# Kernel tuning notes

Hardware: AMD Instinct MI355X
Metric: run time of the kernel (lower is better)

The kernel has to match this reference:

```python
import jax, jax.numpy as jnp
import numpy as np

B, IN, H, M = 16384, 512, 512, 4096


def setup_inputs() -> dict:
    key = jax.random.key(0)
    ks = jax.random.split(key, 8)
    s_in = 1.0 / np.sqrt(IN + H)
    return {
        "input_tensor": jax.random.normal(ks[0], (B, IN), jnp.float32),
        "hidden": jax.random.normal(ks[1], (B, H), jnp.float32),
        "cell": jax.random.normal(ks[2], (B, H), jnp.float32),
        # fused gate weights: columns = [input, forget, cell, output] gates
        "W_gates": jax.random.normal(ks[3], (IN + H, 4 * H), jnp.float32) * s_in,
        "b_gates": jnp.zeros((4 * H,), jnp.float32),
        "W_attn": jax.random.normal(ks[4], (H, M), jnp.float32) / np.sqrt(H),
        "b_attn": jnp.zeros((M,), jnp.float32),
        "memory_matrix": jax.random.normal(ks[5], (M, H), jnp.float32) * np.sqrt(2.0 / (M + H)),
    }


def reference(input_tensor, hidden, cell, W_gates, b_gates, W_attn, b_attn, memory_matrix):
    combined = jnp.concatenate([input_tensor, hidden], axis=1)        # (B, IN+H)
    gates = combined @ W_gates + b_gates                              # (B, 4H)
    i_g, f_g, c_g, o_g = jnp.split(gates, 4, axis=1)
    i_g = jax.nn.sigmoid(i_g)
    f_g = jax.nn.sigmoid(f_g)
    c_g = jnp.tanh(c_g)
    o_g = jax.nn.sigmoid(o_g)
    attn = jax.nn.softmax(hidden @ W_attn + b_attn, axis=1)           # (B, M)
    memory_read = attn @ memory_matrix                                # (B, H)
    new_cell = f_g * cell + i_g * c_g + 0.1 * memory_read
    new_hidden = o_g * jnp.tanh(new_cell)
    return (new_hidden, new_cell, attn)
```

## Files before the change

kernel.cpp:

```cpp
#include <hip/hip_runtime.h>
#include <hip/hip_bf16.h>
#include <math.h>

typedef __bf16 bf16_t;
typedef bf16_t bf16x8 __attribute__((ext_vector_type(8)));
typedef float  f32x4  __attribute__((ext_vector_type(4)));

static constexpr int Bn = 16384;
static constexpr int Hn = 512;

__device__ __forceinline__ float sigm(float x) { return 1.0f / (1.0f + __expf(-x)); }

typedef __attribute__((address_space(3))) void lds_void;
typedef const __attribute__((address_space(1))) void gl_void;

__device__ __forceinline__ void glds16(const void* g, void* l) {
    __builtin_amdgcn_global_load_lds((gl_void*)g, (lds_void*)l, 16, 0, 0);
}

__global__ void convert_comb(const float* __restrict__ inp, const float* __restrict__ hid,
                             bf16_t* __restrict__ comb)
{
    size_t t = (size_t)blockIdx.x * blockDim.x + threadIdx.x;
    size_t r = t >> 7;
    int c8 = (int)(t & 127);
    const float* src = (c8 < 64) ? (inp + r * 512 + c8 * 8) : (hid + r * 512 + (c8 - 64) * 8);
    float4 a = ((const float4*)src)[0];
    float4 b = ((const float4*)src)[1];
    bf16x8 o;
    o[0] = (bf16_t)a.x; o[1] = (bf16_t)a.y; o[2] = (bf16_t)a.z; o[3] = (bf16_t)a.w;
    o[4] = (bf16_t)b.x; o[5] = (bf16_t)b.y; o[6] = (bf16_t)b.z; o[7] = (bf16_t)b.w;
    *(bf16x8*)(comb + t * 8) = o;
}

__global__ void transpose_all(const float* __restrict__ Wg, bf16_t* __restrict__ WgT,
                              const float* __restrict__ Wa, bf16_t* __restrict__ WaT,
                              const float* __restrict__ Mem, bf16_t* __restrict__ MemT)
{
    __shared__ float tile[32][33];
    int b = blockIdx.x;
    const float* src; bf16_t* dst; int R, C, gx;
    if (b < 2048)      { src = Wg;  dst = WgT;  R = 1024; C = 2048; gx = 64; }
    else if (b < 4096) { b -= 2048; src = Wa;  dst = WaT;  R = 512;  C = 4096; gx = 128; }
    else               { b -= 4096; src = Mem; dst = MemT; R = 4096; C = 512;  gx = 16; }
    const int x0 = (b % gx) * 32, y0 = (b / gx) * 32;
    const int tx = threadIdx.x & 31, ty = threadIdx.x >> 5;
#pragma unroll
    for (int i = 0; i < 32; i += 8)
        tile[ty + i][tx] = src[(size_t)(y0 + ty + i) * C + x0 + tx];
    __syncthreads();
#pragma unroll
    for (int i = 0; i < 32; i += 8)
        dst[(size_t)(x0 + ty + i) * R + y0 + tx] = (bf16_t)tile[tx][ty + i];
}

template<int EPI>
__global__ __launch_bounds__(256)
void gemm_k64(const bf16_t* __restrict__ A, int lda,
              const bf16_t* __restrict__ Bt, int ldb,
              const float* __restrict__ bias, int K, int N,
              bf16_t* __restrict__ bout, float* __restrict__ fout,
              const bf16_t* __restrict__ gates, const float* __restrict__ cell)
{
    __shared__ __align__(16) bf16_t sA[128 * 64];
    __shared__ __align__(16) bf16_t sB[128 * 64];

    const int tid = threadIdx.x, lane = tid & 63, wid = tid >> 6;
    const int wr = wid >> 1, wc = wid & 1;

    const int nwg = gridDim.x;
    int bid = blockIdx.x;
    bid = (bid & 7) * (nwg >> 3) + (bid >> 3);
    const int gx = N >> 7;
    const int row0 = (bid / gx) * 128, col0 = (bid % gx) * 128;

    f32x4 acc[4][4] = {};
    const int nk = K >> 6;
    const int l15 = lane & 15, kq = lane >> 4;

    for (int kt = 0; kt < nk; ++kt) {
        const int k0 = kt << 6;
#pragma unroll
        for (int t = 0; t < 4; ++t) {
            const int c8 = wid * 4 + t;
            const int r = c8 * 8 + (lane >> 3);
            const int slot = (lane & 7) ^ (lane >> 3);
            glds16(A + (size_t)(row0 + r) * lda + k0 + slot * 8, sA + c8 * 512);
            glds16(Bt + (size_t)(col0 + r) * ldb + k0 + slot * 8, sB + c8 * 512);
        }
        __syncthreads();

#pragma unroll
        for (int ks = 0; ks < 2; ++ks) {
            bf16x8 af[4], bfr[4];
#pragma unroll
            for (int j = 0; j < 4; ++j) {
                const int rb = wc * 64 + j * 16 + l15;
                const int slot = (ks * 4 + kq) ^ (l15 & 7);
                bfr[j] = *(const bf16x8*)&sB[rb * 64 + slot * 8];
                const int ra = wr * 64 + j * 16 + l15;
                af[j] = *(const bf16x8*)&sA[ra * 64 + slot * 8];
            }
#pragma unroll
            for (int i = 0; i < 4; ++i)
#pragma unroll
                for (int j = 0; j < 4; ++j)
                    acc[i][j] = __builtin_amdgcn_mfma_f32_16x16x32_bf16(af[i], bfr[j], acc[i][j], 0, 0, 0);
        }
        __syncthreads();
    }

    const int lr = (lane >> 4) * 4, lc = lane & 15;
#pragma unroll
    for (int i = 0; i < 4; ++i) {
#pragma unroll
        for (int j = 0; j < 4; ++j) {
#pragma unroll
            for (int r = 0; r < 4; ++r) {
                const int grow = row0 + wr * 64 + i * 16 + lr + r;
                const int gcol = col0 + wc * 64 + j * 16 + lc;
                float v = acc[i][j][r];
                if constexpr (EPI == 0) {
                    v += bias[gcol];
                    const float a = ((gcol >> 9) == 2) ? tanhf(v) : sigm(v);
                    bout[(size_t)grow * 2048 + gcol] = (bf16_t)a;
                } else if constexpr (EPI == 1) {
                    bout[(size_t)grow * 8192 + gcol] = (bf16_t)(v + bias[gcol]);
                } else {
                    const float ig = (float)gates[(size_t)grow * 2048 + gcol];
                    const float fg = (float)gates[(size_t)grow * 2048 + 512 + gcol];
                    const float cg = (float)gates[(size_t)grow * 2048 + 1024 + gcol];
                    const float og = (float)gates[(size_t)grow * 2048 + 1536 + gcol];
                    const float cv = cell[(size_t)grow * 512 + gcol];
                    const float ncv = fg * cv + ig * cg + 0.1f * v;
                    fout[(size_t)grow * 512 + gcol] = og * tanhf(ncv);
                    fout[(size_t)Bn * Hn + (size_t)grow * 512 + gcol] = ncv;
                }
            }
        }
    }
}

__global__ void softmax_mid(float* __restrict__ attn)
{
    const int row = blockIdx.x;
    float* rp = attn + (size_t)row * 4096;
    bf16_t* lp = (bf16_t*)rp;
    const int tid = threadIdx.x;

    float v[16];
    {
        bf16x8 h0 = ((const bf16x8*)lp)[tid];
        bf16x8 h1 = ((const bf16x8*)lp)[tid + 256];
#pragma unroll
        for (int k = 0; k < 8; ++k) { v[k] = (float)h0[k]; v[8 + k] = (float)h1[k]; }
    }
    float mx = v[0];
#pragma unroll
    for (int k = 1; k < 16; ++k) mx = fmaxf(mx, v[k]);
#pragma unroll
    for (int off = 32; off > 0; off >>= 1) mx = fmaxf(mx, __shfl_xor(mx, off));
    __shared__ float smx[4], ssm[4];
    if ((tid & 63) == 0) smx[tid >> 6] = mx;
    __syncthreads();
    mx = fmaxf(fmaxf(smx[0], smx[1]), fmaxf(smx[2], smx[3]));

    float sum = 0.0f;
#pragma unroll
    for (int k = 0; k < 16; ++k) { v[k] = __expf(v[k] - mx); sum += v[k]; }
#pragma unroll
    for (int off = 32; off > 0; off >>= 1) sum += __shfl_xor(sum, off);
    if ((tid & 63) == 0) ssm[tid >> 6] = sum;
    __syncthreads();
    sum = ssm[0] + ssm[1] + ssm[2] + ssm[3];

    const float inv = 1.0f / sum;
    bf16x8 o0, o1;
#pragma unroll
    for (int k = 0; k < 8; ++k) { o0[k] = (bf16_t)(v[k] * inv); o1[k] = (bf16_t)(v[8 + k] * inv); }
    ((bf16x8*)lp)[tid]       = o0;
    ((bf16x8*)lp)[tid + 256] = o1;
}

__global__ void expand_attn(float* __restrict__ attn)
{
    const int row = blockIdx.x;
    float* rp = attn + (size_t)row * 4096;
    const int t = threadIdx.x;
    bf16x8 h0 = ((const bf16x8*)rp)[2 * t];
    bf16x8 h1 = ((const bf16x8*)rp)[2 * t + 1];
    __syncthreads();
    float4 o0 = { (float)h0[0], (float)h0[1], (float)h0[2], (float)h0[3] };
    float4 o1 = { (float)h0[4], (float)h0[5], (float)h0[6], (float)h0[7] };
    float4 o2 = { (float)h1[0], (float)h1[1], (float)h1[2], (float)h1[3] };
    float4 o3 = { (float)h1[4], (float)h1[5], (float)h1[6], (float)h1[7] };
    ((float4*)rp)[4 * t]     = o0;
    ((float4*)rp)[4 * t + 1] = o1;
    ((float4*)rp)[4 * t + 2] = o2;
    ((float4*)rp)[4 * t + 3] = o3;
}

extern "C" void kernel_launch(void* const* d_in, const int* in_sizes, int n_in,
                              void* d_out, int out_size, void* d_ws, size_t ws_size,
                              hipStream_t stream)
{
    const float* input  = (const float*)d_in[0];
    const float* hidden = (const float*)d_in[1];
    const float* cell   = (const float*)d_in[2];
    const float* Wg     = (const float*)d_in[3];
    const float* bg     = (const float*)d_in[4];
    const float* Wa     = (const float*)d_in[5];
    const float* ba     = (const float*)d_in[6];
    const float* Mem    = (const float*)d_in[7];

    float* out  = (float*)d_out;
    float* attn = out + 2ull * Bn * Hn;

    bf16_t* comb  = (bf16_t*)d_ws;
    bf16_t* WgT   = comb + (size_t)Bn * 1024;
    bf16_t* WaT   = WgT + (size_t)2048 * 1024;
    bf16_t* MemT  = WaT + (size_t)4096 * 512;
    bf16_t* gates = MemT + (size_t)512 * 4096;

    convert_comb<<<8192, 256, 0, stream>>>(input, hidden, comb);
    transpose_all<<<6144, 256, 0, stream>>>(Wg, WgT, Wa, WaT, Mem, MemT);

    gemm_k64<0><<<2048, 256, 0, stream>>>(comb, 1024, WgT, 1024, bg, 1024, 2048,
                                          gates, nullptr, nullptr, nullptr);
    gemm_k64<1><<<4096, 256, 0, stream>>>(comb + 512, 1024, WaT, 512, ba, 512, 4096,
                                          (bf16_t*)attn, nullptr, nullptr, nullptr);
    softmax_mid<<<Bn, 256, 0, stream>>>(attn);
    gemm_k64<2><<<512, 256, 0, stream>>>((const bf16_t*)attn, 8192, MemT, 4096, nullptr, 4096, 512,
                                         nullptr, out, gates, cell);
    expand_attn<<<Bn, 256, 0, stream>>>(attn);
}
```

Before: 527.1 us.

## Merge gate and attention GEMMs, write fp32 attn in softmax, retile memory GEMM

Merges the gate GEMM and the attention-logit GEMM into one launch. Column blocks 0-15 compute the gates and 16-47 compute the logits, so one grid covers both with no launch gap in between. When the workspace is big enough, the bf16 softmax result goes to a separate workspace buffer, and softmax writes the fp32 attn output directly, which removes the separate expand pass. The memory-read GEMM now uses 64-row tiles and a 1024-block grid to improve occupancy across CUs. The trade-off is extra workspace use and a branch inside the fused GEMM.

```diff
diff --git a/kernel.cpp b/kernel.cpp
--- a/kernel.cpp
+++ b/kernel.cpp
@@ -54,13 +54,11 @@
         dst[(size_t)(x0 + ty + i) * R + y0 + tx] = (bf16_t)tile[tx][ty + i];
 }
 
-template<int EPI>
 __global__ __launch_bounds__(256)
-void gemm_k64(const bf16_t* __restrict__ A, int lda,
-              const bf16_t* __restrict__ Bt, int ldb,
-              const float* __restrict__ bias, int K, int N,
-              bf16_t* __restrict__ bout, float* __restrict__ fout,
-              const bf16_t* __restrict__ gates, const float* __restrict__ cell)
+void gemm12(const bf16_t* __restrict__ comb,
+            const bf16_t* __restrict__ WgT, const bf16_t* __restrict__ WaT,
+            const float* __restrict__ bg, const float* __restrict__ ba,
+            bf16_t* __restrict__ gates, bf16_t* __restrict__ logit, int lstride)
 {
     __shared__ __align__(16) bf16_t sA[128 * 64];
     __shared__ __align__(16) bf16_t sB[128 * 64];
@@ -68,11 +66,14 @@
     const int tid = threadIdx.x, lane = tid & 63, wid = tid >> 6;
     const int wr = wid >> 1, wc = wid & 1;
 
-    const int nwg = gridDim.x;
-    int bid = blockIdx.x;
-    bid = (bid & 7) * (nwg >> 3) + (bid >> 3);
-    const int gx = N >> 7;
-    const int row0 = (bid / gx) * 128, col0 = (bid % gx) * 128;
+    int bid = (blockIdx.x & 7) * 768 + (blockIdx.x >> 3);
+    const int rb = bid / 48, cb = bid % 48;
+    const bool g = cb < 16;
+    const int K = g ? 1024 : 512;
+    const bf16_t* A  = comb + (g ? 0 : 512);
+    const bf16_t* Bt = g ? WgT : WaT;
+    const int col0 = (g ? cb : cb - 16) * 128;
+    const int row0 = rb * 128;
 
     f32x4 acc[4][4] = {};
     const int nk = K >> 6;
@@ -85,19 +86,18 @@
             const int c8 = wid * 4 + t;
             const int r = c8 * 8 + (lane >> 3);
             const int slot = (lane & 7) ^ (lane >> 3);
-            glds16(A + (size_t)(row0 + r) * lda + k0 + slot * 8, sA + c8 * 512);
-            glds16(Bt + (size_t)(col0 + r) * ldb + k0 + slot * 8, sB + c8 * 512);
+            glds16(A + (size_t)(row0 + r) * 1024 + k0 + slot * 8, sA + c8 * 512);
+            glds16(Bt + (size_t)(col0 + r) * K + k0 + slot * 8, sB + c8 * 512);
         }
         __syncthreads();
-
 #pragma unroll
         for (int ks = 0; ks < 2; ++ks) {
             bf16x8 af[4], bfr[4];
 #pragma unroll
             for (int j = 0; j < 4; ++j) {
-                const int rb = wc * 64 + j * 16 + l15;
+                const int rbq = wc * 64 + j * 16 + l15;
                 const int slot = (ks * 4 + kq) ^ (l15 & 7);
-                bfr[j] = *(const bf16x8*)&sB[rb * 64 + slot * 8];
+                bfr[j] = *(const bf16x8*)&sB[rbq * 64 + slot * 8];
                 const int ra = wr * 64 + j * 16 + l15;
                 af[j] = *(const bf16x8*)&sA[ra * 64 + slot * 8];
             }
@@ -120,32 +120,105 @@
                 const int grow = row0 + wr * 64 + i * 16 + lr + r;
                 const int gcol = col0 + wc * 64 + j * 16 + lc;
                 float v = acc[i][j][r];
-                if constexpr (EPI == 0) {
-                    v += bias[gcol];
+                if (g) {
+                    v += bg[gcol];
                     const float a = ((gcol >> 9) == 2) ? tanhf(v) : sigm(v);
-                    bout[(size_t)grow * 2048 + gcol] = (bf16_t)a;
-                } else if constexpr (EPI == 1) {
-                    bout[(size_t)grow * 8192 + gcol] = (bf16_t)(v + bias[gcol]);
+                    gates[(size_t)grow * 2048 + gcol] = (bf16_t)a;
                 } else {
-                    const float ig = (float)gates[(size_t)grow * 2048 + gcol];
-                    const float fg = (float)gates[(size_t)grow * 2048 + 512 + gcol];
-                    const float cg = (float)gates[(size_t)grow * 2048 + 1024 + gcol];
-                    const float og = (float)gates[(size_t)grow * 2048 + 1536 + gcol];
-                    const float cv = cell[(size_t)grow * 512 + gcol];
-                    const float ncv = fg * cv + ig * cg + 0.1f * v;
-                    fout[(size_t)grow * 512 + gcol] = og * tanhf(ncv);
-                    fout[(size_t)Bn * Hn + (size_t)grow * 512 + gcol] = ncv;
+                    logit[(size_t)grow * lstride + gcol] = (bf16_t)(v + ba[gcol]);
                 }
             }
         }
     }
 }
 
-__global__ void softmax_mid(float* __restrict__ attn)
+__global__ __launch_bounds__(256)
+void gemm3k(const bf16_t* __restrict__ Ap, int astride,
+            const bf16_t* __restrict__ MemT,
+            const bf16_t* __restrict__ gates, const float* __restrict__ cell,
+            float* __restrict__ fout)
+{
+    __shared__ __align__(16) bf16_t sA[64 * 64];
+    __shared__ __align__(16) bf16_t sB[128 * 64];
+
+    const int tid = threadIdx.x, lane = tid & 63, wid = tid >> 6;
+    const int wr = wid >> 1, wc = wid & 1;
+
+    int bid = (blockIdx.x & 7) * 128 + (blockIdx.x >> 3);
+    const int row0 = (bid >> 2) * 64, col0 = (bid & 3) * 128;
+
+    f32x4 acc[2][4] = {};
+    const int l15 = lane & 15, kq = lane >> 4;
+
+    for (int kt = 0; kt < 64; ++kt) {
+        const int k0 = kt << 6;
+#pragma unroll
+        for (int t = 0; t < 2; ++t) {
+            const int c8 = wid * 2 + t;
+            const int r = c8 * 8 + (lane >> 3);
+            const int slot = (lane & 7) ^ (lane >> 3);
+            glds16(Ap + (size_t)(row0 + r) * astride + k0 + slot * 8, sA + c8 * 512);
+        }
+#pragma unroll
+        for (int t = 0; t < 4; ++t) {
+            const int c8 = wid * 4 + t;
+            const int r = c8 * 8 + (lane >> 3);
+            const int slot = (lane & 7) ^ (lane >> 3);
+            glds16(MemT + (size_t)(col0 + r) * 4096 + k0 + slot * 8, sB + c8 * 512);
+        }
+        __syncthreads();
+#pragma unroll
+        for (int ks = 0; ks < 2; ++ks) {
+            bf16x8 af[2], bfr[4];
+#pragma unroll
+            for (int j = 0; j < 4; ++j) {
+                const int rbq = wc * 64 + j * 16 + l15;
+                const int slot = (ks * 4 + kq) ^ (l15 & 7);
+                bfr[j] = *(const bf16x8*)&sB[rbq * 64 + slot * 8];
+            }
+#pragma unroll
+            for (int i = 0; i < 2; ++i) {
+                const int ra = wr * 32 + i * 16 + l15;
+                const int slot = (ks * 4 + kq) ^ (l15 & 7);
+                af[i] = *(const bf16x8*)&sA[ra * 64 + slot * 8];
+            }
+#pragma unroll
+            for (int i = 0; i < 2; ++i)
+#pragma unroll
+                for (int j = 0; j < 4; ++j)
+                    acc[i][j] = __builtin_amdgcn_mfma_f32_16x16x32_bf16(af[i], bfr[j], acc[i][j], 0, 0, 0);
+        }
+        __syncthreads();
+    }
+
+    const int lr = (lane >> 4) * 4, lc = lane & 15;
+#pragma unroll
+    for (int i = 0; i < 2; ++i) {
+#pragma unroll
+        for (int j = 0; j < 4; ++j) {
+#pragma unroll
+            for (int r = 0; r < 4; ++r) {
+                const int grow = row0 + wr * 32 + i * 16 + lr + r;
+                const int gcol = col0 + wc * 64 + j * 16 + lc;
+                const float v = acc[i][j][r];
+                const float ig = (float)gates[(size_t)grow * 2048 + gcol];
+                const float fg = (float)gates[(size_t)grow * 2048 + 512 + gcol];
+                const float cg = (float)gates[(size_t)grow * 2048 + 1024 + gcol];
+                const float og = (float)gates[(size_t)grow * 2048 + 1536 + gcol];
+                const float cv = cell[(size_t)grow * 512 + gcol];
+                const float ncv = fg * cv + ig * cg + 0.1f * v;
+                fout[(size_t)grow * 512 + gcol] = og * tanhf(ncv);
+                fout[(size_t)Bn * Hn + (size_t)grow * 512 + gcol] = ncv;
+            }
+        }
+    }
+}
+
+template<bool F32OUT>
+__global__ void softmax_k(bf16_t* __restrict__ packed, int pstride, float* __restrict__ attnf32)
 {
     const int row = blockIdx.x;
-    float* rp = attn + (size_t)row * 4096;
-    bf16_t* lp = (bf16_t*)rp;
+    bf16_t* lp = packed + (size_t)row * pstride;
     const int tid = threadIdx.x;
 
     float v[16];
@@ -175,11 +248,24 @@
     sum = ssm[0] + ssm[1] + ssm[2] + ssm[3];
 
     const float inv = 1.0f / sum;
+#pragma unroll
+    for (int k = 0; k < 16; ++k) v[k] *= inv;
+
     bf16x8 o0, o1;
 #pragma unroll
-    for (int k = 0; k < 8; ++k) { o0[k] = (bf16_t)(v[k] * inv); o1[k] = (bf16_t)(v[8 + k] * inv); }
+    for (int k = 0; k < 8; ++k) { o0[k] = (bf16_t)v[k]; o1[k] = (bf16_t)v[8 + k]; }
     ((bf16x8*)lp)[tid]       = o0;
     ((bf16x8*)lp)[tid + 256] = o1;
+
+    if constexpr (F32OUT) {
+        float* rp = attnf32 + (size_t)row * 4096;
+        float4 a0 = { v[0], v[1], v[2], v[3] },   a1 = { v[4], v[5], v[6], v[7] };
+        float4 a2 = { v[8], v[9], v[10], v[11] }, a3 = { v[12], v[13], v[14], v[15] };
+        ((float4*)rp)[2 * tid]             = a0;
+        ((float4*)rp)[2 * tid + 1]         = a1;
+        ((float4*)rp)[2 * (tid + 256)]     = a2;
+        ((float4*)rp)[2 * (tid + 256) + 1] = a3;
+    }
 }
 
 __global__ void expand_attn(float* __restrict__ attn)
@@ -221,16 +307,23 @@
     bf16_t* WaT   = WgT + (size_t)2048 * 1024;
     bf16_t* MemT  = WaT + (size_t)4096 * 512;
     bf16_t* gates = MemT + (size_t)512 * 4096;
+    bf16_t* pws   = gates + (size_t)Bn * 2048;
+
+    const size_t need_big = ((size_t)Bn * 1024 + 2048 * 1024 + 4096 * 512 + 512 * 4096
+                             + (size_t)Bn * 2048 + (size_t)Bn * 4096) * sizeof(bf16_t);
+    const bool big = ws_size >= need_big;
+    bf16_t* packed = big ? pws : (bf16_t*)attn;
+    const int pstride = big ? 4096 : 8192;
 
     convert_comb<<<8192, 256, 0, stream>>>(input, hidden, comb);
     transpose_all<<<6144, 256, 0, stream>>>(Wg, WgT, Wa, WaT, Mem, MemT);
 
-    gemm_k64<0><<<2048, 256, 0, stream>>>(comb, 1024, WgT, 1024, bg, 1024, 2048,
-                                          gates, nullptr, nullptr, nullptr);
-    gemm_k64<1><<<4096, 256, 0, stream>>>(comb + 512, 1024, WaT, 512, ba, 512, 4096,
-                                          (bf16_t*)attn, nullptr, nullptr, nullptr);
-    softmax_mid<<<Bn, 256, 0, stream>>>(attn);
-    gemm_k64<2><<<512, 256, 0, stream>>>((const bf16_t*)attn, 8192, MemT, 4096, nullptr, 4096, 512,
-                                         nullptr, out, gates, cell);
-    expand_attn<<<Bn, 256, 0, stream>>>(attn);
-}
+    gemm12<<<6144, 256, 0, stream>>>(comb, WgT, WaT, bg, ba, gates, packed, pstride);
+
+    if (big) softmax_k<true><<<Bn, 256, 0, stream>>>(packed, pstride, attn);
+    else     softmax_k<false><<<Bn, 256, 0, stream>>>(packed, pstride, nullptr);
+
+    gemm3k<<<1024, 256, 0, stream>>>(packed, pstride, MemT, gates, cell, out);
+
+    if (!big) expand_attn<<<Bn, 256, 0, stream>>>(attn);
+}
```

After: 619.8 us. +17.6%, slower.
